# Kernel optimization log

Hardware: AMD Instinct MI355X
Metric: run time of the kernel (lower is better)

Reference implementation:

```python
import jax, jax.numpy as jnp
import numpy as np

EPS = 1e-6

def setup_inputs() -> dict:
    key = jax.random.key(0)
    ks = jax.random.split(key, 8)
    B, S, E, C = 2, 2048, 1024, 256
    x = jax.random.normal(ks[0], (B, S, E), dtype=jnp.float32)
    mask = jnp.triu(jnp.ones((S, S), dtype=bool), k=1)  # True = masked (causal)
    conditioning = jax.random.normal(ks[1], (B, C), dtype=jnp.float32)
    sc = 1.0 / np.sqrt(E)
    Wq = jax.random.normal(ks[2], (E, E), dtype=jnp.float32) * sc
    Wk = jax.random.normal(ks[3], (E, E), dtype=jnp.float32) * sc
    Wv = jax.random.normal(ks[4], (E, E), dtype=jnp.float32) * sc
    Wo = jax.random.normal(ks[5], (E, E), dtype=jnp.float32) * sc
    rms_scale = jnp.ones((E,), dtype=jnp.float32)
    Wc = jax.random.normal(ks[6], (2 * E, C), dtype=jnp.float32) * 0.02
    bc = jax.random.normal(ks[7], (2 * E,), dtype=jnp.float32) * 0.02
    return {"x": x, "mask": mask, "conditioning": conditioning,
            "Wq": Wq, "Wk": Wk, "Wv": Wv, "Wo": Wo,
            "rms_scale": rms_scale, "Wc": Wc, "bc": bc}

def reference(x, mask, conditioning, Wq, Wk, Wv, Wo, rms_scale, Wc, bc):
    B, S, E = x.shape
    H = 16
    D = E // H
    scale = D ** -0.5
    # QKV projections (nn.Linear: x @ W.T), reshape to (B,H,S,D)
    def proj(W):
        return (x @ W.T).reshape(B, S, H, D).transpose(0, 2, 1, 3)
    q, k, v = proj(Wq), proj(Wk), proj(Wv)
    # attention scores (B,H,S,S)
    scores = jnp.einsum('bhsd,bhtd->bhst', q, k) * scale
    scores = jnp.where(mask[None, None, :, :], -jnp.inf, scores)
    attn = jax.nn.softmax(scores, axis=-1)
    out = jnp.einsum('bhst,bhtd->bhsd', attn, v)  # (B,H,S,D)
    out = out.transpose(0, 2, 1, 3).reshape(B, S, E)
    out = out @ Wo.T
    # AdaptiveRMSNorm + FiLM
    rms = jnp.sqrt(jnp.mean(out * out, axis=-1, keepdims=True) + EPS)
    xn = out / rms * rms_scale
    mod = jax.nn.silu(conditioning) @ Wc.T + bc  # (B, 2E)
    shift, sc = jnp.split(mod, 2, axis=-1)
    xn = xn * (1.0 + sc[:, None, :]) + shift[:, None, :]
    return xn
```

## Files before the change

kernel.cpp:

```cpp
#include <hip/hip_runtime.h>
#include <hip/hip_bf16.h>
#include <stdint.h>

typedef __bf16 bf16;
typedef __bf16 bf16x8 __attribute__((ext_vector_type(8)));
typedef float  f32x4  __attribute__((ext_vector_type(4)));

#define NB 2
#define NS 2048
#define NE 1024
#define NH 16
#define ND 64
#define NC 256

#define EXP2(x) __builtin_amdgcn_exp2f(x)

__device__ __forceinline__ void gload16(void* lds, const void* g) {
  __builtin_amdgcn_global_load_lds(
      (const __attribute__((address_space(1))) void*)g,
      (__attribute__((address_space(3))) void*)lds, 16, 0, 0);
}

template <int CTRL>
__device__ __forceinline__ float rowror_max(float x) {
  int xi = __builtin_bit_cast(int, x);
  int yi = __builtin_amdgcn_update_dpp(xi, xi, CTRL, 0xF, 0xF, false);
  return fmaxf(x, __builtin_bit_cast(float, yi));
}

__device__ __forceinline__ float rowmax16(float x) {
  x = rowror_max<0x121>(x);
  x = rowror_max<0x122>(x);
  x = rowror_max<0x124>(x);
  x = rowror_max<0x128>(x);
  return x;
}

__global__ __launch_bounds__(256) void cvt_kernel(
    const float* __restrict__ src, bf16* __restrict__ dst, int n) {
  int i = (blockIdx.x * 256 + threadIdx.x) * 8;
  if (i >= n) return;
  float4 a = ((const float4*)(src + i))[0];
  float4 b = ((const float4*)(src + i))[1];
  bf16x8 o;
  o[0] = (bf16)a.x; o[1] = (bf16)a.y; o[2] = (bf16)a.z; o[3] = (bf16)a.w;
  o[4] = (bf16)b.x; o[5] = (bf16)b.y; o[6] = (bf16)b.z; o[7] = (bf16)b.w;
  *(bf16x8*)(dst + i) = o;
}

__global__ __launch_bounds__(256) void cvt4_kernel(
    const float* __restrict__ s0, const float* __restrict__ s1,
    const float* __restrict__ s2, const float* __restrict__ s3,
    bf16* __restrict__ dst) {
  int seg = blockIdx.x >> 9;
  int blk = blockIdx.x & 511;
  const float* s = (seg == 0) ? s0 : (seg == 1) ? s1 : (seg == 2) ? s2 : s3;
  int i = (blk * 256 + threadIdx.x) * 8;
  float4 a = ((const float4*)(s + i))[0];
  float4 b = ((const float4*)(s + i))[1];
  bf16x8 o;
  o[0] = (bf16)a.x; o[1] = (bf16)a.y; o[2] = (bf16)a.z; o[3] = (bf16)a.w;
  o[4] = (bf16)b.x; o[5] = (bf16)b.y; o[6] = (bf16)b.z; o[7] = (bf16)b.w;
  *(bf16x8*)(dst + seg * 1048576 + i) = o;
}

__global__ __launch_bounds__(256) void mod_kernel(
    const float* __restrict__ cond, const float* __restrict__ Wc,
    const float* __restrict__ bc, float* __restrict__ mod) {
  __shared__ float scond[NC];
  int b  = blockIdx.x >> 3;
  int j0 = (blockIdx.x & 7) * 256;
  float c = cond[b * NC + threadIdx.x];
  scond[threadIdx.x] = c / (1.f + __expf(-c));
  __syncthreads();
  int j = j0 + threadIdx.x;
  float acc = bc[j];
  const float* wrow = Wc + (size_t)j * NC;
  for (int cc = 0; cc < NC; ++cc) acc += scond[cc] * wrow[cc];
  mod[b * 2 * NE + j] = acc;
}

template<int MODE>
__global__ __launch_bounds__(256) void gemm128(
    const bf16* __restrict__ A, const bf16* __restrict__ W0,
    const bf16* __restrict__ W1, const bf16* __restrict__ W2,
    void* __restrict__ out, int K) {
  __shared__ bf16 As[128 * 32];
  __shared__ bf16 Bs[128 * 32];
  const int t = threadIdx.x, w = t >> 6, l = t & 63;
  const int lr = l & 15, lg = l >> 4;
  const int wm = w >> 1, wn = w & 1;
  const int m0 = blockIdx.x * 128;
  const int ng = blockIdx.y * 128;

  const bf16* Bw;
  if (MODE == 0) {
    const bf16* Ws[3] = {W0, W1, W2};
    Bw = Ws[ng >> 10] + (size_t)(ng & 1023) * K;
  } else {
    Bw = W0 + (size_t)ng * K;
  }

  f32x4 acc[4][4];
#pragma unroll
  for (int i = 0; i < 4; ++i)
#pragma unroll
    for (int j = 0; j < 4; ++j) acc[i][j] = (f32x4){0.f, 0.f, 0.f, 0.f};

  const int srow = (l >> 2);
  const int scol = (l & 3) * 8;

  for (int kt = 0; kt < K; kt += 32) {
#pragma unroll
    for (int r = 0; r < 2; ++r) {
      int cc = w * 2 + r;
      int row = cc * 16 + srow;
      gload16((char*)As + cc * 1024, A  + (size_t)(m0 + row) * K + kt + scol);
      gload16((char*)Bs + cc * 1024, Bw + (size_t)row        * K + kt + scol);
    }
    __syncthreads();
    bf16x8 af[4], bfr[4];
#pragma unroll
    for (int i = 0; i < 4; ++i) {
      af[i]  = *(const bf16x8*)(As + (wm * 64 + i * 16 + lr) * 32 + lg * 8);
      bfr[i] = *(const bf16x8*)(Bs + (wn * 64 + i * 16 + lr) * 32 + lg * 8);
    }
#pragma unroll
    for (int i = 0; i < 4; ++i)
#pragma unroll
      for (int j = 0; j < 4; ++j)
        acc[i][j] = __builtin_amdgcn_mfma_f32_16x16x32_bf16(af[i], bfr[j], acc[i][j], 0, 0, 0);
    if (kt + 32 < K) __syncthreads();
  }

#pragma unroll
  for (int i = 0; i < 4; ++i) {
#pragma unroll
    for (int j = 0; j < 4; ++j) {
#pragma unroll
      for (int r = 0; r < 4; ++r) {
        int row = m0 + wm * 64 + i * 16 + lg * 4 + r;
        int col = ng + wn * 64 + j * 16 + lr;
        float v = acc[i][j][r];
        if (MODE == 1) {
          ((float*)out)[(size_t)row * NE + col] = v;
        } else {
          int b = row >> 11, s = row & 2047;
          int wi = col >> 10, nc = col & 1023;
          int h = nc >> 6, d = nc & 63;
          size_t hb = (size_t)(b * NH + h) * 131072u;
          size_t idx;
          if (wi == 0) v *= 0.180336880f;
          if (wi == 2)
            idx = 8388608u + hb +
                  (size_t)((d >> 4) * 32768 + (s >> 3) * 128 + (d & 15) * 8 + (s & 7));
          else
            idx = (size_t)wi * 4194304u + hb +
                  (size_t)((s >> 4) * 1024 + (d >> 3) * 128 + (s & 15) * 8 + (d & 7));
          ((bf16*)out)[idx] = (bf16)v;
        }
      }
    }
  }
}

__global__ __launch_bounds__(256, 4) void attn_kernel(
    const bf16* __restrict__ Q, const bf16* __restrict__ Km,
    const bf16* __restrict__ Vt, bf16* __restrict__ O) {
  __shared__ float smrg[4][24][64];
  const int l = threadIdx.x & 63, w = threadIdx.x >> 6;
  const int lr = l & 15, lg = l >> 4;
  const int bid = blockIdx.x;
  const int xcd = bid & 7, slot = bid >> 3;
  const int bh = xcd * 4 + (slot >> 5);
  const int b = bh >> 4, h = bh & 15;
  const int sl = slot & 31;
  const int tp = sl * 2 + (w >> 1);
  const int hw = w & 1;

  bf16* pb = (bf16*)&smrg[w][0][0];

  const bf16* Qh = Q  + (size_t)bh * 131072u + l * 8;
  const bf16* Kh = Km + (size_t)bh * 131072u + l * 8;
  const bf16* Vh = Vt + (size_t)bh * 131072u + l * 8;

  bf16x8 ones;
#pragma unroll
  for (int i = 0; i < 8; ++i) ones[i] = (bf16)1.0f;

  for (int pass = 0; pass < 2; ++pass) {
    const int qbase = (pass ? (127 - tp) : tp) * 16;

    bf16x8 qf0 = *(const bf16x8*)(Qh + (qbase >> 4) * 1024);
    bf16x8 qf1 = *(const bf16x8*)(Qh + (qbase >> 4) * 1024 + 512);

    f32x4 o[4], osum;
#pragma unroll
    for (int dt = 0; dt < 4; ++dt) o[dt] = (f32x4){0.f, 0.f, 0.f, 0.f};
    osum = (f32x4){0.f, 0.f, 0.f, 0.f};
    float mrow[4];
    int qr[4];
#pragma unroll
    for (int r = 0; r < 4; ++r) { mrow[r] = -1e30f; qr[r] = qbase + lg * 4 + r; }

    for (int kv0 = hw * 64; kv0 < qbase + 16; kv0 += 128) {
      const bf16* kt = Kh + (kv0 >> 4) * 1024;
      const bf16* vt = Vh + (kv0 >> 3) * 128;
      bf16x8 k0[4], k1[4], v0[4], v1[4];
#pragma unroll
      for (int nt = 0; nt < 4; ++nt) {
        k0[nt] = *(const bf16x8*)(kt + nt * 1024);
        k1[nt] = *(const bf16x8*)(kt + nt * 1024 + 512);
      }
#pragma unroll
      for (int dt = 0; dt < 4; ++dt) {
        v0[dt] = *(const bf16x8*)(vt + dt * 32768);
        v1[dt] = *(const bf16x8*)(vt + dt * 32768 + 512);
      }
      f32x4 s[4];
#pragma unroll
      for (int nt = 0; nt < 4; ++nt) {
        f32x4 z = (f32x4){0.f, 0.f, 0.f, 0.f};
        z = __builtin_amdgcn_mfma_f32_16x16x32_bf16(qf0, k0[nt], z, 0, 0, 0);
        z = __builtin_amdgcn_mfma_f32_16x16x32_bf16(qf1, k1[nt], z, 0, 0, 0);
        s[nt] = z;
      }
      const bool edge = (kv0 + 63 > qbase);
      float pm[4];
#pragma unroll
      for (int r = 0; r < 4; ++r) pm[r] = -1e30f;
#pragma unroll
      for (int nt = 0; nt < 4; ++nt) {
        f32x4 v = s[nt];
#pragma unroll
        for (int r = 0; r < 4; ++r) {
          if (edge && (kv0 + nt * 16 + lr > qr[r])) v[r] = -1e30f;
          pm[r] = fmaxf(pm[r], v[r]);
        }
        s[nt] = v;
      }
#pragma unroll
      for (int r = 0; r < 4; ++r) pm[r] = rowmax16(pm[r]);
      float al[4];
#pragma unroll
      for (int r = 0; r < 4; ++r) {
        float nm = fmaxf(mrow[r], pm[r]);
        al[r] = EXP2(mrow[r] - nm);
        mrow[r] = nm;
      }
#pragma unroll
      for (int dt = 0; dt < 4; ++dt)
#pragma unroll
        for (int r = 0; r < 4; ++r) o[dt][r] *= al[r];
#pragma unroll
      for (int r = 0; r < 4; ++r) osum[r] *= al[r];
#pragma unroll
      for (int nt = 0; nt < 4; ++nt)
#pragma unroll
        for (int r = 0; r < 4; ++r)
          pb[(lg * 4 + r) * 72 + nt * 16 + lr] = (bf16)EXP2(s[nt][r] - mrow[r]);
      asm volatile("s_waitcnt lgkmcnt(0)" ::: "memory");
      __builtin_amdgcn_sched_barrier(0);
      bf16x8 pa0 = *(const bf16x8*)(pb + lr * 72 + lg * 8);
      bf16x8 pa1 = *(const bf16x8*)(pb + lr * 72 + 32 + lg * 8);
      osum = __builtin_amdgcn_mfma_f32_16x16x32_bf16(pa0, ones, osum, 0, 0, 0);
      osum = __builtin_amdgcn_mfma_f32_16x16x32_bf16(pa1, ones, osum, 0, 0, 0);
#pragma unroll
      for (int dt = 0; dt < 4; ++dt) {
        o[dt] = __builtin_amdgcn_mfma_f32_16x16x32_bf16(pa0, v0[dt], o[dt], 0, 0, 0);
        o[dt] = __builtin_amdgcn_mfma_f32_16x16x32_bf16(pa1, v1[dt], o[dt], 0, 0, 0);
      }
      __builtin_amdgcn_sched_barrier(0);
    }

    float* my = &smrg[w][0][0];
#pragma unroll
    for (int r = 0; r < 4; ++r) { my[r * 64 + l] = mrow[r]; my[(4 + r) * 64 + l] = osum[r]; }
#pragma unroll
    for (int dt = 0; dt < 4; ++dt)
#pragma unroll
      for (int r = 0; r < 4; ++r) my[(8 + dt * 4 + r) * 64 + l] = o[dt][r];
    __syncthreads();

    const float* pt = &smrg[w ^ 1][0][0];
    float sS[4], sP[4], rl[4];
#pragma unroll
    for (int r = 0; r < 4; ++r) {
      float mp = pt[r * 64 + l];
      float mm = fmaxf(mrow[r], mp);
      sS[r] = EXP2(mrow[r] - mm);
      sP[r] = EXP2(mp - mm);
      float lsum = sS[r] * osum[r] + sP[r] * pt[(4 + r) * 64 + l];
      rl[r] = 1.f / lsum;
    }
#pragma unroll
    for (int dd = 0; dd < 2; ++dd) {
      const int dt = hw * 2 + dd;
#pragma unroll
      for (int r = 0; r < 4; ++r) {
        float val = sS[r] * o[dt][r] + sP[r] * pt[(8 + dt * 4 + r) * 64 + l];
        O[((size_t)(b * NS) + qr[r]) * NE + h * ND + dt * 16 + lr] =
            (bf16)(val * rl[r]);
      }
    }
    __syncthreads();
  }
}

__global__ __launch_bounds__(256) void norm_kernel(
    const float* __restrict__ tmp, const float* __restrict__ rms_scale,
    const float* __restrict__ mod, float* __restrict__ out) {
  int row = blockIdx.x;
  int b = row >> 11;
  const float* trow = tmp + (size_t)row * NE;
  float4 v = ((const float4*)trow)[threadIdx.x];
  float vv[4] = {v.x, v.y, v.z, v.w};
  float ss = vv[0]*vv[0] + vv[1]*vv[1] + vv[2]*vv[2] + vv[3]*vv[3];
#pragma unroll
  for (int mk = 1; mk < 64; mk <<= 1) ss += __shfl_xor(ss, mk, 64);
  __shared__ float sred[4];
  if ((threadIdx.x & 63) == 0) sred[threadIdx.x >> 6] = ss;
  __syncthreads();
  float tot = sred[0] + sred[1] + sred[2] + sred[3];
  float rinv = rsqrtf(tot * (1.f / NE) + 1e-6f);
  const float* modb = mod + b * 2 * NE;
#pragma unroll
  for (int j = 0; j < 4; ++j) {
    int e = threadIdx.x * 4 + j;
    float xn = vv[j] * rinv * rms_scale[e];
    xn = xn * (1.f + modb[NE + e]) + modb[e];
    out[(size_t)row * NE + e] = xn;
  }
}

extern "C" void kernel_launch(void* const* d_in, const int* in_sizes, int n_in,
                              void* d_out, int out_size, void* d_ws, size_t ws_size,
                              hipStream_t stream) {
  const float* x    = (const float*)d_in[0];
  const float* cond = (const float*)d_in[2];
  const float* Wq   = (const float*)d_in[3];
  const float* Wk   = (const float*)d_in[4];
  const float* Wv   = (const float*)d_in[5];
  const float* Wo   = (const float*)d_in[6];
  const float* rmss = (const float*)d_in[7];
  const float* Wc   = (const float*)d_in[8];
  const float* bc   = (const float*)d_in[9];
  float* out = (float*)d_out;

  char* ws = (char*)d_ws;
  const size_t MB = 1u << 20;
  bf16*  xb  = (bf16*)(ws);
  bf16*  Wqb = (bf16*)(ws + 8  * MB);
  bf16*  Wkb = (bf16*)(ws + 10 * MB);
  bf16*  Wvb = (bf16*)(ws + 12 * MB);
  bf16*  Wob = (bf16*)(ws + 14 * MB);
  bf16*  Qb  = (bf16*)(ws + 16 * MB);
  bf16*  Kb  = (bf16*)(ws + 24 * MB);
  bf16*  Vt  = (bf16*)(ws + 32 * MB);
  bf16*  Oa  = (bf16*)(ws);
  float* tmp = (float*)(ws + 16 * MB);
  float* mod = (float*)(ws + 40 * MB);

  const int NX = NB * NS * NE;

  mod_kernel<<<16, 256, 0, stream>>>(cond, Wc, bc, mod);

  cvt_kernel<<<NX / 2048, 256, 0, stream>>>(x, xb, NX);
  cvt4_kernel<<<2048, 256, 0, stream>>>(Wq, Wk, Wv, Wo, Wqb);

  gemm128<0><<<dim3(32, 24), 256, 0, stream>>>(xb, Wqb, Wkb, Wvb, Qb, NE);

  attn_kernel<<<1024, 256, 0, stream>>>(Qb, Kb, Vt, Oa);

  gemm128<1><<<dim3(32, 8), 256, 0, stream>>>(Oa, Wob, nullptr, nullptr, tmp, NE);

  norm_kernel<<<NB * NS, 256, 0, stream>>>(tmp, rmss, mod, out);
}
```

Baseline: 138.8 us.

## Merge conversion kernels, store out-proj as bf16, add lazy softmax rescale

```diff
diff --git a/kernel.cpp b/kernel.cpp
--- a/kernel.cpp
+++ b/kernel.cpp
@@ -3,6 +3,7 @@
 #include <stdint.h>
 
 typedef __bf16 bf16;
+typedef __bf16 bf16x4 __attribute__((ext_vector_type(4)));
 typedef __bf16 bf16x8 __attribute__((ext_vector_type(8)));
 typedef float  f32x4  __attribute__((ext_vector_type(4)));
 
@@ -36,32 +37,27 @@
   return x;
 }
 
-__global__ __launch_bounds__(256) void cvt_kernel(
-    const float* __restrict__ src, bf16* __restrict__ dst, int n) {
-  int i = (blockIdx.x * 256 + threadIdx.x) * 8;
-  if (i >= n) return;
-  float4 a = ((const float4*)(src + i))[0];
-  float4 b = ((const float4*)(src + i))[1];
-  bf16x8 o;
-  o[0] = (bf16)a.x; o[1] = (bf16)a.y; o[2] = (bf16)a.z; o[3] = (bf16)a.w;
-  o[4] = (bf16)b.x; o[5] = (bf16)b.y; o[6] = (bf16)b.z; o[7] = (bf16)b.w;
-  *(bf16x8*)(dst + i) = o;
-}
-
-__global__ __launch_bounds__(256) void cvt4_kernel(
-    const float* __restrict__ s0, const float* __restrict__ s1,
-    const float* __restrict__ s2, const float* __restrict__ s3,
-    bf16* __restrict__ dst) {
-  int seg = blockIdx.x >> 9;
-  int blk = blockIdx.x & 511;
-  const float* s = (seg == 0) ? s0 : (seg == 1) ? s1 : (seg == 2) ? s2 : s3;
-  int i = (blk * 256 + threadIdx.x) * 8;
+__global__ __launch_bounds__(256) void cvt_all_kernel(
+    const float* __restrict__ x,  const float* __restrict__ w0,
+    const float* __restrict__ w1, const float* __restrict__ w2,
+    const float* __restrict__ w3, bf16* __restrict__ xb,
+    bf16* __restrict__ wb) {
+  int blk = blockIdx.x;
+  const float* s; bf16* d; int off;
+  if (blk < 2048) {
+    s = x; d = xb; off = blk * 2048;
+  } else {
+    int seg = (blk - 2048) >> 9, bb = (blk - 2048) & 511;
+    const float* ws[4] = {w0, w1, w2, w3};
+    s = ws[seg]; d = wb + seg * 1048576; off = bb * 2048;
+  }
+  int i = off + threadIdx.x * 8;
   float4 a = ((const float4*)(s + i))[0];
   float4 b = ((const float4*)(s + i))[1];
   bf16x8 o;
   o[0] = (bf16)a.x; o[1] = (bf16)a.y; o[2] = (bf16)a.z; o[3] = (bf16)a.w;
   o[4] = (bf16)b.x; o[5] = (bf16)b.y; o[6] = (bf16)b.z; o[7] = (bf16)b.w;
-  *(bf16x8*)(dst + seg * 1048576 + i) = o;
+  *(bf16x8*)(d + i) = o;
 }
 
 __global__ __launch_bounds__(256) void mod_kernel(
@@ -143,7 +139,7 @@
         int col = ng + wn * 64 + j * 16 + lr;
         float v = acc[i][j][r];
         if (MODE == 1) {
-          ((float*)out)[(size_t)row * NE + col] = v;
+          ((bf16*)out)[(size_t)row * NE + col] = (bf16)v;
         } else {
           int b = row >> 11, s = row & 2047;
           int wi = col >> 10, nc = col & 1023;
@@ -241,19 +237,24 @@
       }
 #pragma unroll
       for (int r = 0; r < 4; ++r) pm[r] = rowmax16(pm[r]);
-      float al[4];
-#pragma unroll
-      for (int r = 0; r < 4; ++r) {
-        float nm = fmaxf(mrow[r], pm[r]);
-        al[r] = EXP2(mrow[r] - nm);
-        mrow[r] = nm;
-      }
-#pragma unroll
-      for (int dt = 0; dt < 4; ++dt)
-#pragma unroll
-        for (int r = 0; r < 4; ++r) o[dt][r] *= al[r];
-#pragma unroll
-      for (int r = 0; r < 4; ++r) osum[r] *= al[r];
+      int grow = 0;
+#pragma unroll
+      for (int r = 0; r < 4; ++r) grow |= (pm[r] > mrow[r] + 8.f);
+      if (__any(grow)) {
+        float al[4];
+#pragma unroll
+        for (int r = 0; r < 4; ++r) {
+          float nm = fmaxf(mrow[r], pm[r]);
+          al[r] = EXP2(mrow[r] - nm);
+          mrow[r] = nm;
+        }
+#pragma unroll
+        for (int dt = 0; dt < 4; ++dt)
+#pragma unroll
+          for (int r = 0; r < 4; ++r) o[dt][r] *= al[r];
+#pragma unroll
+        for (int r = 0; r < 4; ++r) osum[r] *= al[r];
+      }
 #pragma unroll
       for (int nt = 0; nt < 4; ++nt)
 #pragma unroll
@@ -270,7 +271,6 @@
         o[dt] = __builtin_amdgcn_mfma_f32_16x16x32_bf16(pa0, v0[dt], o[dt], 0, 0, 0);
         o[dt] = __builtin_amdgcn_mfma_f32_16x16x32_bf16(pa1, v1[dt], o[dt], 0, 0, 0);
       }
-      __builtin_amdgcn_sched_barrier(0);
     }
 
     float* my = &smrg[w][0][0];
@@ -308,13 +308,13 @@
 }
 
 __global__ __launch_bounds__(256) void norm_kernel(
-    const float* __restrict__ tmp, const float* __restrict__ rms_scale,
+    const bf16* __restrict__ tmp, const float* __restrict__ rms_scale,
     const float* __restrict__ mod, float* __restrict__ out) {
   int row = blockIdx.x;
   int b = row >> 11;
-  const float* trow = tmp + (size_t)row * NE;
-  float4 v = ((const float4*)trow)[threadIdx.x];
-  float vv[4] = {v.x, v.y, v.z, v.w};
+  const bf16* trow = tmp + (size_t)row * NE;
+  bf16x4 v = ((const bf16x4*)trow)[threadIdx.x];
+  float vv[4] = {(float)v[0], (float)v[1], (float)v[2], (float)v[3]};
   float ss = vv[0]*vv[0] + vv[1]*vv[1] + vv[2]*vv[2] + vv[3]*vv[3];
 #pragma unroll
   for (int mk = 1; mk < 64; mk <<= 1) ss += __shfl_xor(ss, mk, 64);
@@ -351,24 +351,19 @@
   const size_t MB = 1u << 20;
   bf16*  xb  = (bf16*)(ws);
   bf16*  Wqb = (bf16*)(ws + 8  * MB);
-  bf16*  Wkb = (bf16*)(ws + 10 * MB);
-  bf16*  Wvb = (bf16*)(ws + 12 * MB);
   bf16*  Wob = (bf16*)(ws + 14 * MB);
   bf16*  Qb  = (bf16*)(ws + 16 * MB);
   bf16*  Kb  = (bf16*)(ws + 24 * MB);
   bf16*  Vt  = (bf16*)(ws + 32 * MB);
   bf16*  Oa  = (bf16*)(ws);
-  float* tmp = (float*)(ws + 16 * MB);
+  bf16*  tmp = (bf16*)(ws + 16 * MB);
   float* mod = (float*)(ws + 40 * MB);
 
-  const int NX = NB * NS * NE;
-
   mod_kernel<<<16, 256, 0, stream>>>(cond, Wc, bc, mod);
 
-  cvt_kernel<<<NX / 2048, 256, 0, stream>>>(x, xb, NX);
-  cvt4_kernel<<<2048, 256, 0, stream>>>(Wq, Wk, Wv, Wo, Wqb);
-
-  gemm128<0><<<dim3(32, 24), 256, 0, stream>>>(xb, Wqb, Wkb, Wvb, Qb, NE);
+  cvt_all_kernel<<<4096, 256, 0, stream>>>(x, Wq, Wk, Wv, Wo, xb, Wqb);
+
+  gemm128<0><<<dim3(32, 24), 256, 0, stream>>>(xb, Wqb, Wqb + 1048576, Wqb + 2097152, Qb, NE);
 
   attn_kernel<<<1024, 256, 0, stream>>>(Qb, Kb, Vt, Oa);
 
```

After: 134.8 us. -2.9%, faster.
